# Kernel tuning notes

Hardware: AMD Instinct MI355X
Metric: run time of the kernel (lower is better)

Reference implementation:

```python
import jax, jax.numpy as jnp
import numpy as np

IN_NC = 512

def setup_inputs() -> dict:
    key = jax.random.key(0)
    k1, k2, k3, k4 = jax.random.split(key, 4)
    B, N = 8, 2048
    nd, out_nc = 512, 512
    x = jax.random.normal(k1, (B, N * IN_NC), dtype=jnp.float32)
    # store weights as [in_nc, d] so projection is x @ W (same math as torch Linear with W^T)
    Wq = jax.random.normal(k2, (IN_NC, nd), dtype=jnp.float32) * (1.0 / np.sqrt(IN_NC))
    Wk = jax.random.normal(k3, (IN_NC, nd), dtype=jnp.float32) * (1.0 / np.sqrt(IN_NC))
    Wv = jax.random.normal(k4, (IN_NC, out_nc), dtype=jnp.float32) * (1.0 / np.sqrt(IN_NC))
    return {"x": x, "Wq": Wq, "Wk": Wk, "Wv": Wv}

def reference(x, Wq, Wk, Wv):
    B = x.shape[0]
    N = x.shape[1] // IN_NC
    xt = x.reshape(B, N, IN_NC)                     # [B, N, in_nc]
    Q = jnp.einsum('bnc,cd->bnd', xt, Wq)           # [B, N, nd]
    K = jnp.einsum('bnc,cd->bnd', xt, Wk)           # [B, N, nd]
    V = jnp.einsum('bnc,cd->bnd', xt, Wv)           # [B, N, out_nc]
    A = jnp.einsum('bnd,bmd->bnm', Q, K)            # [B, N, N]  (no scale, as in source)
    A = jax.nn.softmax(A, axis=-1)
    out = jnp.einsum('bnm,bmd->bnd', A, V)          # [B, N, out_nc]
    return out.reshape(B, -1)
```

## Files before the change

kernel.cpp:

```cpp
#include <hip/hip_runtime.h>
#include <hip/hip_fp16.h>

typedef _Float16 f16x8 __attribute__((ext_vector_type(8)));
typedef _Float16 f16x4 __attribute__((ext_vector_type(4)));
typedef float    f32x4 __attribute__((ext_vector_type(4)));

#define LOG2E 1.44269504f

__device__ __forceinline__ void stage128x64(const _Float16* __restrict__ g, int ld,
                                            void* lds, int tid)
{
    const int r0   = tid >> 3;
    const int colh = ((tid & 7) ^ (r0 & 7)) << 3;
    char* lbase = (char*)lds + (tid >> 6) * 1024;
#pragma unroll
    for (int i = 0; i < 4; i++) {
        const _Float16* src = g + (size_t)(i * 32 + r0) * ld + colh;
        __builtin_amdgcn_global_load_lds(
            (const __attribute__((address_space(1))) void*)src,
            (__attribute__((address_space(3))) void*)(lbase + i * 4096),
            16, 0, 0);
    }
}

__device__ __forceinline__ f16x8 lds_frag(const void* lds, int row, int colh)
{
    const int off = row * 128 + ((colh * 2) ^ ((row & 7) << 4));
    return *(const f16x8*)((const char*)lds + off);
}

template<int NK>
__device__ __forceinline__ void gemm_loop_cv(const _Float16* __restrict__ A, int lda,
                                             const _Float16* __restrict__ B, int ldb,
                                             _Float16* a0, _Float16* a1,
                                             _Float16* b0, _Float16* b1,
                                             f32x4 acc[4][4], int tid,
                                             int wr, int wc, int lrow, int lkg)
{
    stage128x64(A, lda, a0, tid);
    stage128x64(B, ldb, b0, tid);
    stage128x64(A + 64, lda, a1, tid);
    stage128x64(B + 64, ldb, b1, tid);
    asm volatile("s_waitcnt vmcnt(8)" ::: "memory");
    __builtin_amdgcn_s_barrier();
    __builtin_amdgcn_sched_barrier(0);

    for (int t = 0; t < NK; ++t) {
        _Float16* acur = (t & 1) ? a1 : a0;
        _Float16* bcur = (t & 1) ? b1 : b0;

        f16x8 af[2][4], bf[2][4];
#pragma unroll
        for (int kk = 0; kk < 2; kk++) {
#pragma unroll
            for (int mi = 0; mi < 4; mi++)
                af[kk][mi] = lds_frag(acur, wr * 64 + mi * 16 + lrow, kk * 32 + lkg * 8);
#pragma unroll
            for (int ni = 0; ni < 4; ni++)
                bf[kk][ni] = lds_frag(bcur, wc * 64 + ni * 16 + lrow, kk * 32 + lkg * 8);
        }
        asm volatile("s_waitcnt lgkmcnt(0)" ::: "memory");
        __builtin_amdgcn_sched_barrier(0);
        __builtin_amdgcn_s_barrier();

        if (t + 2 < NK) {
            stage128x64(A + (size_t)(t + 2) * 64, lda, acur, tid);
            stage128x64(B + (size_t)(t + 2) * 64, ldb, bcur, tid);
        }
        __builtin_amdgcn_sched_barrier(0);

        __builtin_amdgcn_s_setprio(1);
#pragma unroll
        for (int kk = 0; kk < 2; kk++)
#pragma unroll
            for (int mi = 0; mi < 4; mi++)
#pragma unroll
                for (int ni = 0; ni < 4; ni++)
                    acc[mi][ni] = __builtin_amdgcn_mfma_f32_16x16x32_f16(
                        af[kk][mi], bf[kk][ni], acc[mi][ni], 0, 0, 0);
        __builtin_amdgcn_s_setprio(0);

        if (t + 2 < NK) asm volatile("s_waitcnt vmcnt(8)" ::: "memory");
        else            asm volatile("s_waitcnt vmcnt(0)" ::: "memory");
        __builtin_amdgcn_sched_barrier(0);
        __builtin_amdgcn_s_barrier();
        __builtin_amdgcn_sched_barrier(0);
    }
}

__global__ __launch_bounds__(256)
void convert_kernel(const float* __restrict__ x,
                    const float* __restrict__ Wq,
                    const float* __restrict__ Wk,
                    const float* __restrict__ Wv,
                    _Float16* __restrict__ xh,
                    _Float16* __restrict__ Wt)
{
    const int b = blockIdx.x;
    if (b < 2048) {
        const size_t base = (size_t)b * 4096 + (size_t)threadIdx.x * 4;
#pragma unroll
        for (int i = 0; i < 4; i++) {
            f32x4 v = *(const f32x4*)(x + base + i * 1024);
            f16x4 h;
#pragma unroll
            for (int j = 0; j < 4; j++) h[j] = (_Float16)v[j];
            *(f16x4*)(xh + base + i * 1024) = h;
        }
    } else {
        __shared__ float tb[32][33];
        const int t = b - 2048;
        const int mat = t >> 8;
        const int tile = t & 255;
        const int tr = tile >> 4, tc = tile & 15;
        const float* W = (mat == 0) ? Wq : (mat == 1) ? Wk : Wv;
        const int r = threadIdx.x >> 5, c = threadIdx.x & 31;
#pragma unroll
        for (int p = 0; p < 4; p++)
            tb[p * 8 + r][c] = W[(size_t)(tr * 32 + p * 8 + r) * 512 + tc * 32 + c];
        __syncthreads();
#pragma unroll
        for (int p = 0; p < 4; p++)
            Wt[((size_t)mat * 512 + tc * 32 + p * 8 + r) * 512 + tr * 32 + c] =
                (_Float16)tb[c][p * 8 + r];
    }
}

__global__ __launch_bounds__(256, 2)
void proj_kernel(const _Float16* __restrict__ xh,
                 const _Float16* __restrict__ Wt,
                 _Float16* __restrict__ Qf,
                 _Float16* __restrict__ Kf,
                 _Float16* __restrict__ Vt)
{
    __shared__ _Float16 a0[128 * 64], a1[128 * 64];
    __shared__ _Float16 b0[128 * 64], b1[128 * 64];

    const int tid = threadIdx.x;
    const int mb = blockIdx.x, cb = blockIdx.y;
    const int mat = cb >> 2, nb = cb & 3;
    const int m0 = mb * 128, n0 = nb * 128;

    const _Float16* Abase = xh + (size_t)m0 * 512;
    const _Float16* Bbase = Wt + ((size_t)mat * 512 + n0) * 512;

    const int lane = tid & 63;
    const int w = tid >> 6;
    const int wr = w >> 1, wc = w & 1;
    const int lrow = lane & 15, lkg = lane >> 4;

    f32x4 acc[4][4];
#pragma unroll
    for (int i = 0; i < 4; i++)
#pragma unroll
        for (int j = 0; j < 4; j++) acc[i][j] = (f32x4)0.0f;

    gemm_loop_cv<8>(Abase, 512, Bbase, 512, a0, a1, b0, b1,
                    acc, tid, wr, wc, lrow, lkg);

    if (mat < 2) {
        _Float16* Out = (mat == 0) ? Qf : Kf;
#pragma unroll
        for (int mi = 0; mi < 4; mi++) {
            const int mbase = m0 + wr * 64 + mi * 16 + lkg * 4;
#pragma unroll
            for (int ni = 0; ni < 4; ni++) {
                const int ncol = n0 + wc * 64 + ni * 16 + lrow;
#pragma unroll
                for (int r = 0; r < 4; r++)
                    Out[(size_t)(mbase + r) * 512 + ncol] = (_Float16)acc[mi][ni][r];
            }
        }
    } else {
#pragma unroll
        for (int mi = 0; mi < 4; mi++) {
            const int mglob = m0 + wr * 64 + mi * 16 + lkg * 4;
            const int b = mglob >> 11, mloc = mglob & 2047;
#pragma unroll
            for (int ni = 0; ni < 4; ni++) {
                const int d = n0 + wc * 64 + ni * 16 + lrow;
                f16x4 h;
#pragma unroll
                for (int r = 0; r < 4; r++) h[r] = (_Float16)acc[mi][ni][r];
                *(f16x4*)&Vt[((size_t)b * 512 + d) * 2048 + mloc] = h;
            }
        }
    }
}

__global__ __launch_bounds__(256, 2)
void score_kernel(const _Float16* __restrict__ Qf,
                  const _Float16* __restrict__ Kf,
                  _Float16* __restrict__ P,
                  float2* __restrict__ ML, int b0)
{
    __shared__ __align__(16) char smem[65536];
    _Float16* a0  = (_Float16*)smem;
    _Float16* a1  = (_Float16*)(smem + 16384);
    _Float16* b0p = (_Float16*)(smem + 32768);
    _Float16* b1p = (_Float16*)(smem + 49152);
    float (*S_lds)[132] = (float(*)[132])smem;

    const int tid = threadIdx.x;
    const int mb = blockIdx.x, nb = blockIdx.y, bl = blockIdx.z;
    const int bg = b0 + bl;

    const _Float16* Abase = Qf + (size_t)(bg * 2048 + nb * 128) * 512;
    const _Float16* Bbase = Kf + (size_t)(bg * 2048 + mb * 128) * 512;

    const int lane = tid & 63;
    const int w = tid >> 6;
    const int wr = w >> 1, wc = w & 1;
    const int lrow = lane & 15, lkg = lane >> 4;

    f32x4 acc[4][4];
#pragma unroll
    for (int i = 0; i < 4; i++)
#pragma unroll
        for (int j = 0; j < 4; j++) acc[i][j] = (f32x4)0.0f;

    gemm_loop_cv<8>(Abase, 512, Bbase, 512, a0, a1, b0p, b1p,
                    acc, tid, wr, wc, lrow, lkg);

    _Float16* Pb = P + (size_t)bl * 2048 * 2048;
    const int s  = tid >> 2;
    const int c0 = (tid & 3) * 32;

#pragma unroll
    for (int hp = 0; hp < 2; hp++) {
#pragma unroll
        for (int m2 = 0; m2 < 2; m2++) {
            const int mi = hp * 2 + m2;
            const int srow = wr * 32 + m2 * 16 + lkg * 4;
#pragma unroll
            for (int ni = 0; ni < 4; ni++) {
                const int col = wc * 64 + ni * 16 + lrow;
#pragma unroll
                for (int rr = 0; rr < 4; rr++)
                    S_lds[srow + rr][col] = acc[mi][ni][rr];
            }
        }
        __syncthreads();

        f32x4 vv[8];
#pragma unroll
        for (int j = 0; j < 8; j++)
            vv[j] = *(const f32x4*)&S_lds[s][c0 + j * 4];

        float m = vv[0][0];
#pragma unroll
        for (int j = 0; j < 8; j++)
#pragma unroll
            for (int jj = 0; jj < 4; jj++) m = fmaxf(m, vv[j][jj]);
        m = fmaxf(m, __shfl_xor(m, 1));
        m = fmaxf(m, __shfl_xor(m, 2));

        float l = 0.0f;
#pragma unroll
        for (int j = 0; j < 8; j++)
#pragma unroll
            for (int jj = 0; jj < 4; jj++) {
                float e = exp2f((vv[j][jj] - m) * LOG2E);
                vv[j][jj] = e;
                l += e;
            }
        l += __shfl_xor(l, 1);
        l += __shfl_xor(l, 2);

        const int q_local = (s >> 5) * 64 + hp * 32 + (s & 31);
        const int q = nb * 128 + q_local;

        if ((tid & 3) == 0) {
            float2 v; v.x = m; v.y = l;
            ML[((size_t)bl * 2048 + q) * 16 + mb] = v;
        }

#pragma unroll
        for (int j = 0; j < 4; j++) {
            f16x8 h;
#pragma unroll
            for (int jj = 0; jj < 8; jj++) {
                const int idx = j * 8 + jj;
                h[jj] = (_Float16)vv[idx >> 2][idx & 3];
            }
            *(f16x8*)&Pb[(size_t)q * 2048 + mb * 128 + c0 + j * 8] = h;
        }
        __syncthreads();
    }
}

__global__ __launch_bounds__(256, 2)
void out_kernel(const _Float16* __restrict__ P,
                const _Float16* __restrict__ Vt,
                const float2* __restrict__ ML,
                float* __restrict__ out, int b0)
{
    __shared__ _Float16 a0[128 * 64], a1[128 * 64];
    __shared__ _Float16 b0p[128 * 64], b1p[128 * 64];
    __shared__ float scale_lds[128][17];

    const int tid = threadIdx.x;
    const int db = blockIdx.x >> 4, nb = blockIdx.x & 15, bl = blockIdx.y;
    const int bg = b0 + bl;

    if (tid < 128) {
        const float2* mlrow = ML + ((size_t)bl * 2048 + nb * 128 + tid) * 16;
        float2 ml[16];
        float M = -3.4e38f;
#pragma unroll
        for (int t = 0; t < 16; t++) { ml[t] = mlrow[t]; M = fmaxf(M, ml[t].x); }
        float L = 0.0f;
#pragma unroll
        for (int t = 0; t < 16; t++) L += ml[t].y * exp2f((ml[t].x - M) * LOG2E);
        const float invL = 1.0f / L;
#pragma unroll
        for (int t = 0; t < 16; t++)
            scale_lds[tid][t] = exp2f((ml[t].x - M) * LOG2E) * invL;
    }

    const _Float16* Abase = P  + (size_t)bl * 2048 * 2048 + (size_t)(nb * 128) * 2048;
    const _Float16* Bbase = Vt + (size_t)bg * 512  * 2048 + (size_t)(db * 128) * 2048;

    const int lane = tid & 63;
    const int w = tid >> 6;
    const int wr = w >> 1, wc = w & 1;
    const int lrow = lane & 15, lkg = lane >> 4;

    f32x4 acc[4][4];
#pragma unroll
    for (int i = 0; i < 4; i++)
#pragma unroll
        for (int j = 0; j < 4; j++) acc[i][j] = (f32x4)0.0f;

    __syncthreads();

    stage128x64(Abase,      2048, a0,  tid);
    stage128x64(Bbase,      2048, b0p, tid);
    stage128x64(Abase + 64, 2048, a1,  tid);
    stage128x64(Bbase + 64, 2048, b1p, tid);
    asm volatile("s_waitcnt vmcnt(8)" ::: "memory");
    __builtin_amdgcn_s_barrier();
    __builtin_amdgcn_sched_barrier(0);

    for (int t = 0; t < 32; ++t) {
        _Float16* acur = (t & 1) ? a1 : a0;
        _Float16* bcur = (t & 1) ? b1p : b0p;
        const int kt = t >> 1;

        f16x8 af[2][4], bf[2][4];
        float sc[4];
#pragma unroll
        for (int kk = 0; kk < 2; kk++) {
#pragma unroll
            for (int mi = 0; mi < 4; mi++)
                af[kk][mi] = lds_frag(acur, wr * 64 + mi * 16 + lrow, kk * 32 + lkg * 8);
#pragma unroll
            for (int ni = 0; ni < 4; ni++)
                bf[kk][ni] = lds_frag(bcur, wc * 64 + ni * 16 + lrow, kk * 32 + lkg * 8);
        }
#pragma unroll
        for (int mi = 0; mi < 4; mi++)
            sc[mi] = scale_lds[wr * 64 + mi * 16 + lrow][kt];
        asm volatile("s_waitcnt lgkmcnt(0)" ::: "memory");
        __builtin_amdgcn_sched_barrier(0);
        __builtin_amdgcn_s_barrier();

        if (t + 2 < 32) {
            stage128x64(Abase + (size_t)(t + 2) * 64, 2048, acur, tid);
            stage128x64(Bbase + (size_t)(t + 2) * 64, 2048, bcur, tid);
        }
        __builtin_amdgcn_sched_barrier(0);

        __builtin_amdgcn_s_setprio(1);
#pragma unroll
        for (int kk = 0; kk < 2; kk++)
#pragma unroll
            for (int mi = 0; mi < 4; mi++) {
                const f16x8 a = af[kk][mi] * (_Float16)sc[mi];
#pragma unroll
                for (int ni = 0; ni < 4; ni++)
                    acc[mi][ni] = __builtin_amdgcn_mfma_f32_16x16x32_f16(
                        a, bf[kk][ni], acc[mi][ni], 0, 0, 0);
            }
        __builtin_amdgcn_s_setprio(0);

        if (t + 2 < 32) asm volatile("s_waitcnt vmcnt(8)" ::: "memory");
        else            asm volatile("s_waitcnt vmcnt(0)" ::: "memory");
        __builtin_amdgcn_sched_barrier(0);
        __builtin_amdgcn_s_barrier();
        __builtin_amdgcn_sched_barrier(0);
    }

#pragma unroll
    for (int mi = 0; mi < 4; mi++) {
        const int nbase = nb * 128 + wr * 64 + mi * 16 + lkg * 4;
#pragma unroll
        for (int ni = 0; ni < 4; ni++) {
            const int d = db * 128 + wc * 64 + ni * 16 + lrow;
#pragma unroll
            for (int rr = 0; rr < 4; rr++)
                out[((size_t)bg * 2048 + nbase + rr) * 512 + d] = acc[mi][ni][rr];
        }
    }
}

extern "C" void kernel_launch(void* const* d_in, const int* in_sizes, int n_in,
                              void* d_out, int out_size, void* d_ws, size_t ws_size,
                              hipStream_t stream) {
    const float* x  = (const float*)d_in[0];
    const float* Wq = (const float*)d_in[1];
    const float* Wk = (const float*)d_in[2];
    const float* Wv = (const float*)d_in[3];

    const size_t MB = 1024ull * 1024ull;
    char* ws = (char*)d_ws;
    _Float16* Qf = (_Float16*)ws;
    _Float16* Kf = Qf + (size_t)16384 * 512;
    _Float16* Vt = Kf + (size_t)16384 * 512;
    _Float16* P  = Vt + (size_t)16384 * 512;
    float*    out = (float*)d_out;

    int chunk;
    if      (ws_size >= 120 * MB) chunk = 8;
    else if (ws_size >= 88  * MB) chunk = 4;
    else if (ws_size >= 70  * MB) chunk = 2;
    else                          chunk = 1;

    float2* ML = (float2*)(P + (size_t)chunk * 2048 * 2048);

    _Float16* xh = (_Float16*)P;
    _Float16* Wt = xh + (size_t)16384 * 512;

    convert_kernel<<<2816, 256, 0, stream>>>(x, Wq, Wk, Wv, xh, Wt);
    proj_kernel<<<dim3(128, 12), 256, 0, stream>>>(xh, Wt, Qf, Kf, Vt);

    for (int b0 = 0; b0 < 8; b0 += chunk) {
        score_kernel<<<dim3(16, 16, chunk), 256, 0, stream>>>(Qf, Kf, P, ML, b0);
        out_kernel<<<dim3(64, chunk), 256, 0, stream>>>(P, Vt, ML, out, b0);
    }
}
```

Measured before the change: 142.0 us.

## Prefetch next LDS fragments into registers while MFMAs run on current tile

Restructures the GEMM main loops in the projection, score and output kernels to double-buffer register fragments. The next k-tile's LDS reads, and in the output kernel its softmax scale values, are issued before the current tile's MFMAs, so LDS latency overlaps with matrix math instead of stalling each iteration. The global-to-LDS wait and barrier move to the top of the loop. To make room for the second fragment set, the occupancy hint of 2 is dropped from the launch bounds, which raises register pressure and may lower occupancy.

```diff
diff --git a/kernel.cpp b/kernel.cpp
--- a/kernel.cpp
+++ b/kernel.cpp
@@ -29,8 +29,36 @@
     return *(const f16x8*)((const char*)lds + off);
 }
 
+struct Frags { f16x8 a[2][4]; f16x8 b[2][4]; };
+
+__device__ __forceinline__ void read_frags(const void* a_lds, const void* b_lds,
+                                           Frags& f, int wr, int wc, int lrow, int lkg)
+{
+#pragma unroll
+    for (int kk = 0; kk < 2; kk++) {
+#pragma unroll
+        for (int mi = 0; mi < 4; mi++)
+            f.a[kk][mi] = lds_frag(a_lds, wr * 64 + mi * 16 + lrow, kk * 32 + lkg * 8);
+#pragma unroll
+        for (int ni = 0; ni < 4; ni++)
+            f.b[kk][ni] = lds_frag(b_lds, wc * 64 + ni * 16 + lrow, kk * 32 + lkg * 8);
+    }
+}
+
+__device__ __forceinline__ void mfma_frags(const Frags& f, f32x4 acc[4][4])
+{
+#pragma unroll
+    for (int kk = 0; kk < 2; kk++)
+#pragma unroll
+        for (int mi = 0; mi < 4; mi++)
+#pragma unroll
+            for (int ni = 0; ni < 4; ni++)
+                acc[mi][ni] = __builtin_amdgcn_mfma_f32_16x16x32_f16(
+                    f.a[kk][mi], f.b[kk][ni], acc[mi][ni], 0, 0, 0);
+}
+
 template<int NK>
-__device__ __forceinline__ void gemm_loop_cv(const _Float16* __restrict__ A, int lda,
+__device__ __forceinline__ void gemm_loop_pf(const _Float16* __restrict__ A, int lda,
                                              const _Float16* __restrict__ B, int ldb,
                                              _Float16* a0, _Float16* a1,
                                              _Float16* b0, _Float16* b1,
@@ -45,46 +73,38 @@
     __builtin_amdgcn_s_barrier();
     __builtin_amdgcn_sched_barrier(0);
 
+    Frags f0, f1;
+    read_frags(a0, b0, f0, wr, wc, lrow, lkg);
+
+#pragma unroll 2
     for (int t = 0; t < NK; ++t) {
-        _Float16* acur = (t & 1) ? a1 : a0;
-        _Float16* bcur = (t & 1) ? b1 : b0;
-
-        f16x8 af[2][4], bf[2][4];
-#pragma unroll
-        for (int kk = 0; kk < 2; kk++) {
-#pragma unroll
-            for (int mi = 0; mi < 4; mi++)
-                af[kk][mi] = lds_frag(acur, wr * 64 + mi * 16 + lrow, kk * 32 + lkg * 8);
-#pragma unroll
-            for (int ni = 0; ni < 4; ni++)
-                bf[kk][ni] = lds_frag(bcur, wc * 64 + ni * 16 + lrow, kk * 32 + lkg * 8);
-        }
+        _Float16* cura = (t & 1) ? a1 : a0;
+        _Float16* curb = (t & 1) ? b1 : b0;
+        _Float16* nxta = (t & 1) ? a0 : a1;
+        _Float16* nxtb = (t & 1) ? b0 : b1;
+        Frags& fc = (t & 1) ? f1 : f0;
+        Frags& fn = (t & 1) ? f0 : f1;
+
         asm volatile("s_waitcnt lgkmcnt(0)" ::: "memory");
         __builtin_amdgcn_sched_barrier(0);
         __builtin_amdgcn_s_barrier();
 
         if (t + 2 < NK) {
-            stage128x64(A + (size_t)(t + 2) * 64, lda, acur, tid);
-            stage128x64(B + (size_t)(t + 2) * 64, ldb, bcur, tid);
-        }
+            stage128x64(A + (size_t)(t + 2) * 64, lda, cura, tid);
+            stage128x64(B + (size_t)(t + 2) * 64, ldb, curb, tid);
+            asm volatile("s_waitcnt vmcnt(8)" ::: "memory");
+        } else if (t + 1 < NK) {
+            asm volatile("s_waitcnt vmcnt(0)" ::: "memory");
+        }
+        __builtin_amdgcn_sched_barrier(0);
+        __builtin_amdgcn_s_barrier();
+        if (t + 1 < NK)
+            read_frags(nxta, nxtb, fn, wr, wc, lrow, lkg);
         __builtin_amdgcn_sched_barrier(0);
 
         __builtin_amdgcn_s_setprio(1);
-#pragma unroll
-        for (int kk = 0; kk < 2; kk++)
-#pragma unroll
-            for (int mi = 0; mi < 4; mi++)
-#pragma unroll
-                for (int ni = 0; ni < 4; ni++)
-                    acc[mi][ni] = __builtin_amdgcn_mfma_f32_16x16x32_f16(
-                        af[kk][mi], bf[kk][ni], acc[mi][ni], 0, 0, 0);
+        mfma_frags(fc, acc);
         __builtin_amdgcn_s_setprio(0);
-
-        if (t + 2 < NK) asm volatile("s_waitcnt vmcnt(8)" ::: "memory");
-        else            asm volatile("s_waitcnt vmcnt(0)" ::: "memory");
-        __builtin_amdgcn_sched_barrier(0);
-        __builtin_amdgcn_s_barrier();
-        __builtin_amdgcn_sched_barrier(0);
     }
 }
 
@@ -126,7 +146,7 @@
     }
 }
 
-__global__ __launch_bounds__(256, 2)
+__global__ __launch_bounds__(256)
 void proj_kernel(const _Float16* __restrict__ xh,
                  const _Float16* __restrict__ Wt,
                  _Float16* __restrict__ Qf,
@@ -155,7 +175,7 @@
 #pragma unroll
         for (int j = 0; j < 4; j++) acc[i][j] = (f32x4)0.0f;
 
-    gemm_loop_cv<8>(Abase, 512, Bbase, 512, a0, a1, b0, b1,
+    gemm_loop_pf<8>(Abase, 512, Bbase, 512, a0, a1, b0, b1,
                     acc, tid, wr, wc, lrow, lkg);
 
     if (mat < 2) {
@@ -188,7 +208,7 @@
     }
 }
 
-__global__ __launch_bounds__(256, 2)
+__global__ __launch_bounds__(256)
 void score_kernel(const _Float16* __restrict__ Qf,
                   const _Float16* __restrict__ Kf,
                   _Float16* __restrict__ P,
@@ -219,7 +239,7 @@
 #pragma unroll
         for (int j = 0; j < 4; j++) acc[i][j] = (f32x4)0.0f;
 
-    gemm_loop_cv<8>(Abase, 512, Bbase, 512, a0, a1, b0p, b1p,
+    gemm_loop_pf<8>(Abase, 512, Bbase, 512, a0, a1, b0p, b1p,
                     acc, tid, wr, wc, lrow, lkg);
 
     _Float16* Pb = P + (size_t)bl * 2048 * 2048;
@@ -289,7 +309,7 @@
     }
 }
 
-__global__ __launch_bounds__(256, 2)
+__global__ __launch_bounds__(256)
 void out_kernel(const _Float16* __restrict__ P,
                 const _Float16* __restrict__ Vt,
                 const float2* __restrict__ ML,
@@ -342,32 +362,41 @@
     __builtin_amdgcn_s_barrier();
     __builtin_amdgcn_sched_barrier(0);
 
+    Frags f0, f1;
+    float sc0[4], sc1[4];
+    read_frags(a0, b0p, f0, wr, wc, lrow, lkg);
+#pragma unroll
+    for (int mi = 0; mi < 4; mi++) sc0[mi] = scale_lds[wr * 64 + mi * 16 + lrow][0];
+
+#pragma unroll 2
     for (int t = 0; t < 32; ++t) {
-        _Float16* acur = (t & 1) ? a1 : a0;
-        _Float16* bcur = (t & 1) ? b1p : b0p;
-        const int kt = t >> 1;
-
-        f16x8 af[2][4], bf[2][4];
-        float sc[4];
-#pragma unroll
-        for (int kk = 0; kk < 2; kk++) {
+        _Float16* cura = (t & 1) ? a1 : a0;
+        _Float16* curb = (t & 1) ? b1p : b0p;
+        _Float16* nxta = (t & 1) ? a0 : a1;
+        _Float16* nxtb = (t & 1) ? b0p : b1p;
+        Frags& fc = (t & 1) ? f1 : f0;
+        Frags& fn = (t & 1) ? f0 : f1;
+        float (&scc)[4] = (t & 1) ? sc1 : sc0;
+        float (&scn)[4] = (t & 1) ? sc0 : sc1;
+
+        asm volatile("s_waitcnt lgkmcnt(0)" ::: "memory");
+        __builtin_amdgcn_sched_barrier(0);
+        __builtin_amdgcn_s_barrier();
+
+        if (t + 2 < 32) {
+            stage128x64(Abase + (size_t)(t + 2) * 64, 2048, cura, tid);
+            stage128x64(Bbase + (size_t)(t + 2) * 64, 2048, curb, tid);
+            asm volatile("s_waitcnt vmcnt(8)" ::: "memory");
+        } else if (t + 1 < 32) {
+            asm volatile("s_waitcnt vmcnt(0)" ::: "memory");
+        }
+        __builtin_amdgcn_sched_barrier(0);
+        __builtin_amdgcn_s_barrier();
+        if (t + 1 < 32) {
+            read_frags(nxta, nxtb, fn, wr, wc, lrow, lkg);
 #pragma unroll
             for (int mi = 0; mi < 4; mi++)
-                af[kk][mi] = lds_frag(acur, wr * 64 + mi * 16 + lrow, kk * 32 + lkg * 8);
-#pragma unroll
-            for (int ni = 0; ni < 4; ni++)
-                bf[kk][ni] = lds_frag(bcur, wc * 64 + ni * 16 + lrow, kk * 32 + lkg * 8);
-        }
-#pragma unroll
-        for (int mi = 0; mi < 4; mi++)
-            sc[mi] = scale_lds[wr * 64 + mi * 16 + lrow][kt];
-        asm volatile("s_waitcnt lgkmcnt(0)" ::: "memory");
-        __builtin_amdgcn_sched_barrier(0);
-        __builtin_amdgcn_s_barrier();
-
-        if (t + 2 < 32) {
-            stage128x64(Abase + (size_t)(t + 2) * 64, 2048, acur, tid);
-            stage128x64(Bbase + (size_t)(t + 2) * 64, 2048, bcur, tid);
+                scn[mi] = scale_lds[wr * 64 + mi * 16 + lrow][(t + 1) >> 1];
         }
         __builtin_amdgcn_sched_barrier(0);
 
@@ -376,19 +405,13 @@
         for (int kk = 0; kk < 2; kk++)
 #pragma unroll
             for (int mi = 0; mi < 4; mi++) {
-                const f16x8 a = af[kk][mi] * (_Float16)sc[mi];
+                const f16x8 a = fc.a[kk][mi] * (_Float16)scc[mi];
 #pragma unroll
                 for (int ni = 0; ni < 4; ni++)
                     acc[mi][ni] = __builtin_amdgcn_mfma_f32_16x16x32_f16(
-                        a, bf[kk][ni], acc[mi][ni], 0, 0, 0);
+                        a, fc.b[kk][ni], acc[mi][ni], 0, 0, 0);
             }
         __builtin_amdgcn_s_setprio(0);
-
-        if (t + 2 < 32) asm volatile("s_waitcnt vmcnt(8)" ::: "memory");
-        else            asm volatile("s_waitcnt vmcnt(0)" ::: "memory");
-        __builtin_amdgcn_sched_barrier(0);
-        __builtin_amdgcn_s_barrier();
-        __builtin_amdgcn_sched_barrier(0);
     }
 
 #pragma unroll
```

New measurement: 197.8 us. 39.3% more time.
